# Kernel tuning notes

Hardware: AMD Instinct MI355X
Metric: run time of the kernel (lower is better)

The kernel has to match this reference:

```python
import jax, jax.numpy as jnp
import numpy as np

NUM_HEADS = 16
CHUNK = 64
RMS_EPS = 1.1920928955078125e-07  # torch.finfo(float32).eps, F.rms_norm default


def setup_inputs() -> dict:
    key = jax.random.key(0)
    k1, k2, k3 = jax.random.split(key, 3)
    B, S, D = 2, 4096, 2048
    x = jax.random.normal(k1, (B, S, D), dtype=jnp.float32)
    w_in = jax.random.normal(k2, (5 * D, D), dtype=jnp.float32) * 0.02
    w_out = jax.random.normal(k3, (D, D), dtype=jnp.float32) * 0.02
    return {"x": x, "w_in": w_in, "w_out": w_out}


def _forward(x, w_in, w_out):
    B, S, D = x.shape
    H, hd, C = NUM_HEADS, D // NUM_HEADS, CHUNK
    proj = x @ w_in.T                              # [B,S,5D]
    q, k, v, a, g = jnp.split(proj, 5, axis=-1)
    rs = lambda t: t.reshape(B, S, H, hd)
    q, k, v, a, g = map(rs, (q, k, v, a, g))
    # rms_norm over head_dim, no learned weight
    q = q * jax.lax.rsqrt(jnp.mean(q * q, axis=-1, keepdims=True) + RMS_EPS)
    k = jnp.tanh(k)
    a = jnp.clip(jax.nn.sigmoid(a + 2.0), 0.6, 0.9995)
    u = k * v                                      # updates, float32
    NC = S // C
    # [NC, B, C, H, hd] so lax.scan iterates over chunks
    a_r = a.reshape(B, NC, C, H, hd).transpose(1, 0, 2, 3, 4)
    u_r = u.reshape(B, NC, C, H, hd).transpose(1, 0, 2, 3, 4)

    def step(state, au):
        a_c, u_c = au                              # [B,C,H,hd]
        prefix = jnp.cumprod(a_c, axis=1)
        acc = jnp.cumsum(u_c / jnp.maximum(prefix, 1e-6), axis=1)
        states = prefix * (state[:, None] + acc)   # [B,C,H,hd]
        return states[:, -1], states

    state0 = jnp.zeros((B, H, hd), dtype=jnp.float32)
    _, mem = jax.lax.scan(step, state0, (a_r, u_r))  # [NC,B,C,H,hd]
    memory = mem.transpose(1, 0, 2, 3, 4).reshape(B, S, H, hd)
    gate = jax.nn.sigmoid(g)
    y = gate * (q * memory) + (1.0 - gate) * v
    return y.reshape(B, S, D) @ w_out.T


def reference(x, w_in, w_out):
    return _forward(x, w_in, w_out)
```

## Files before the change

### kernel.cpp

```cpp
#include <hip/hip_runtime.h>
#include <cstdint>
#include <cstddef>

typedef unsigned short u16;
typedef __bf16 bf16x8 __attribute__((ext_vector_type(8)));
typedef unsigned int u32;
typedef u32 u32x4 __attribute__((ext_vector_type(4)));
typedef float f32x4v __attribute__((ext_vector_type(4)));

#define BB 2
#define SS 4096
#define DD 2048
#define HH 16
#define HD 128
#define CC 64
#define NC 64
#define D5 10240
#define RMS_EPS 1.1920928955078125e-07f

__device__ __forceinline__ u16 f2bf(float f) {
  uint32_t x = __float_as_uint(f);
  uint32_t r = (x + 0x7fffu + ((x >> 16) & 1u)) >> 16;
  return (u16)r;
}
__device__ __forceinline__ float bf2f(u16 u) {
  return __uint_as_float(((uint32_t)u) << 16);
}
__device__ __forceinline__ float fast_sigmoid(float x) {
  return 1.0f / (1.0f + __expf(-x));
}
__device__ __forceinline__ float fast_tanh(float x) {
  return 1.0f - 2.0f / (__expf(2.0f * x) + 1.0f);
}

__global__ void cvt_bf16x8_kernel(const f32x4v* __restrict__ src,
                                  u32x4* __restrict__ dst, int n8) {
  int i = blockIdx.x * blockDim.x + threadIdx.x;
  int stride = gridDim.x * blockDim.x;
  for (; i < n8; i += stride) {
    f32x4v a = src[2 * i];
    f32x4v b = src[2 * i + 1];
    u32x4 o;
    o.x = (u32)f2bf(a.x) | ((u32)f2bf(a.y) << 16);
    o.y = (u32)f2bf(a.z) | ((u32)f2bf(a.w) << 16);
    o.z = (u32)f2bf(b.x) | ((u32)f2bf(b.y) << 16);
    o.w = (u32)f2bf(b.z) | ((u32)f2bf(b.w) << 16);
    dst[i] = o;
  }
}

template <typename OutT>
__global__ __launch_bounds__(512, 2) void gemm_bt(const u16* __restrict__ A,
                                                  const u16* __restrict__ B,
                                                  OutT* __restrict__ C,
                                                  int M, int N, int K) {
  __shared__ u16 lds[65536];

  const int tid = threadIdx.x;
  const int wave = tid >> 6;
  const int lane = tid & 63;

  const int nwg = (int)gridDim.x;
  const int bid = (int)blockIdx.x;
  const int bswz = (bid & 7) * (nwg >> 3) + (bid >> 3);
  const int Mt = M >> 8;
  const int m0 = (bswz % Mt) << 8;
  const int n0 = (bswz / Mt) << 8;

  const int wm = (wave >> 2) << 7;
  const int wn = (wave & 3) << 6;

  const int s_r = tid >> 3;
  const int s_ls = (tid & 7) ^ (s_r & 7);
  const u16* Ast = A + (size_t)(m0 + s_r) * K + s_ls * 8;
  const u16* Bst = B + (size_t)(n0 + s_r) * K + s_ls * 8;
  const int s_lb = wave * 512;

  const int fr = lane & 15;
  const int fg = lane >> 4;
  const int fx = lane & 7;
  const int psk0 = ((0 + fg) ^ fx) * 8;
  const int psk1 = ((4 + fg) ^ fx) * 8;
  const int aro = (wm + fr) * 64;
  const int bro = 16384 + (wn + fr) * 64;

  f32x4v acc[8][4] = {};
  bf16x8 afr[4][2];
  bf16x8 bfr[2][2][2];
  const int NT = K >> 6;

#define BARF()                              \
  do {                                      \
    asm volatile("" ::: "memory");          \
    __builtin_amdgcn_s_barrier();           \
    asm volatile("" ::: "memory");          \
  } while (0)

#define STAGE(GB, LB, H, KT)                                                    \
  do {                                                                          \
    const u16* g_ = (GB) + (size_t)((H) * 128) * K + (KT) * 64;                 \
    __builtin_amdgcn_global_load_lds(                                           \
        (__attribute__((address_space(1))) void*)(u16*)g_,                      \
        (__attribute__((address_space(3))) void*)&lds[(LB) + (H) * 8192 + s_lb],\
        16, 0, 0);                                                              \
    __builtin_amdgcn_global_load_lds(                                           \
        (__attribute__((address_space(1))) void*)(u16*)(g_ + (size_t)64 * K),   \
        (__attribute__((address_space(3))) void*)&lds[(LB) + (H) * 8192 + 4096 + s_lb], \
        16, 0, 0);                                                              \
  } while (0)

#define LOADA(BO, MH)                                             \
  do {                                                            \
    _Pragma("unroll") for (int mf = 0; mf < 4; ++mf) {            \
      const int ab_ = (BO) + aro + (MH) * 4096 + mf * 1024;       \
      afr[mf][0] = *(const bf16x8*)&lds[ab_ + psk0];              \
      afr[mf][1] = *(const bf16x8*)&lds[ab_ + psk1];              \
    }                                                             \
  } while (0)

#define LOADB(BO, NH)                                             \
  do {                                                            \
    _Pragma("unroll") for (int nf = 0; nf < 2; ++nf) {            \
      const int bb_ = (BO) + bro + (NH) * 2048 + nf * 1024;       \
      bfr[NH][nf][0] = *(const bf16x8*)&lds[bb_ + psk0];          \
      bfr[NH][nf][1] = *(const bf16x8*)&lds[bb_ + psk1];          \
    }                                                             \
  } while (0)

#define MMAQ(MH, NH)                                                          \
  do {                                                                        \
    __builtin_amdgcn_s_setprio(1);                                            \
    _Pragma("unroll") for (int mf = 0; mf < 4; ++mf)                          \
        _Pragma("unroll") for (int nf = 0; nf < 2; ++nf) {                    \
      acc[(MH) * 4 + mf][(NH) * 2 + nf] =                                     \
          __builtin_amdgcn_mfma_f32_16x16x32_bf16(                            \
              afr[mf][0], bfr[NH][nf][0], acc[(MH) * 4 + mf][(NH) * 2 + nf],  \
              0, 0, 0);                                                       \
      acc[(MH) * 4 + mf][(NH) * 2 + nf] =                                     \
          __builtin_amdgcn_mfma_f32_16x16x32_bf16(                            \
              afr[mf][1], bfr[NH][nf][1], acc[(MH) * 4 + mf][(NH) * 2 + nf],  \
              0, 0, 0);                                                       \
    }                                                                         \
    __builtin_amdgcn_s_setprio(0);                                            \
  } while (0)

  STAGE(Ast, 0, 0, 0);
  STAGE(Ast, 0, 1, 0);
  STAGE(Bst, 16384, 0, 0);
  STAGE(Bst, 16384, 1, 0);
  {
    const int k1 = (NT > 1) ? 1 : 0;
    STAGE(Ast, 32768, 0, k1);
    STAGE(Ast, 32768, 1, k1);
    STAGE(Bst, 49152, 0, k1);
    STAGE(Bst, 49152, 1, k1);
  }
  asm volatile("s_waitcnt vmcnt(8)" ::: "memory");
  BARF();

  for (int t = 0; t < NT; ++t) {
    const int bo = (t & 1) << 15;
    const int t2 = (t + 2 < NT) ? t + 2 : NT - 1;

    LOADA(bo, 0);
    LOADB(bo, 0);
    LOADB(bo, 1);
    MMAQ(0, 0);
    MMAQ(0, 1);
    LOADA(bo, 1);
    MMAQ(1, 1);
    __builtin_amdgcn_sched_barrier(0);
    BARF();

    STAGE(Ast, bo, 0, t2);
    STAGE(Bst, bo + 16384, 0, t2);
    STAGE(Ast, bo, 1, t2);
    STAGE(Bst, bo + 16384, 1, t2);
    MMAQ(1, 0);
    asm volatile("s_waitcnt vmcnt(8)" ::: "memory");
    BARF();
  }

  asm volatile("s_waitcnt vmcnt(0)" ::: "memory");
  BARF();

  const int ccol = lane & 15;
  const int crow = (lane >> 4) << 2;
  if constexpr (sizeof(OutT) == 2) {
    u16* wlds = &lds[wave * 8192];
#pragma unroll
    for (int am = 0; am < 8; ++am) {
#pragma unroll
      for (int an = 0; an < 4; ++an) {
        const int col = ((an >> 1) << 5) + ((an & 1) << 4) + ccol;
        const int cch = col >> 3, cre = col & 7;
#pragma unroll
        for (int r = 0; r < 4; ++r) {
          const int row = ((am >> 2) << 6) + ((am & 3) << 4) + crow + r;
          wlds[row * 64 + ((cch ^ (row & 7)) << 3) + cre] =
              f2bf(acc[am][an][r]);
        }
      }
    }
#pragma unroll
    for (int i = 0; i < 16; ++i) {
      const int row = i * 8 + (lane >> 3);
      const int ch = lane & 7;
      const u32x4 vv = *(const u32x4*)&wlds[row * 64 + (((ch) ^ (row & 7)) << 3)];
      *(u32x4*)(C + (size_t)(m0 + wm + row) * N + (n0 + wn + ch * 8)) = vv;
    }
  } else {
#pragma unroll
    for (int am = 0; am < 8; ++am) {
      const size_t r0 = (size_t)(m0 + wm + ((am >> 2) << 6) + ((am & 3) << 4) + crow);
#pragma unroll
      for (int an = 0; an < 4; ++an) {
        const size_t c0 = (size_t)(n0 + wn + ((an >> 1) << 5) + ((an & 1) << 4) + ccol);
#pragma unroll
        for (int r = 0; r < 4; ++r) {
          OutT* Cp = C + (r0 + r) * (size_t)N + c0;
          *Cp = acc[am][an][r];
        }
      }
    }
  }
#undef BARF
#undef STAGE
#undef LOADA
#undef LOADB
#undef MMAQ
}

__global__ __launch_bounds__(64) void scan_chunk(const u16* __restrict__ proj,
                                                 float* __restrict__ Pc,
                                                 float* __restrict__ Lc) {
  const int idx = blockIdx.x;
  const int h = idx & (HH - 1);
  const int c = (idx >> 4) & (NC - 1);
  const int b = idx >> 10;
  const int lane = threadIdx.x;

  const size_t row0 = (size_t)(b * SS + c * CC) * D5 + h * HD;

  float p0 = 1.0f, a0 = 0.0f, p1 = 1.0f, a1 = 0.0f;
  for (int t = 0; t < CC; ++t) {
    const size_t rp = row0 + (size_t)t * D5;
    float k0 = bf2f(proj[rp + DD + lane]);
    float k1 = bf2f(proj[rp + DD + lane + 64]);
    float v0 = bf2f(proj[rp + 2 * DD + lane]);
    float v1 = bf2f(proj[rp + 2 * DD + lane + 64]);
    float ar0 = bf2f(proj[rp + 3 * DD + lane]);
    float ar1 = bf2f(proj[rp + 3 * DD + lane + 64]);
    float aa0 = fminf(fmaxf(fast_sigmoid(ar0 + 2.0f), 0.6f), 0.9995f);
    float aa1 = fminf(fmaxf(fast_sigmoid(ar1 + 2.0f), 0.6f), 0.9995f);
    p0 *= aa0;
    p1 *= aa1;
    a0 += fast_tanh(k0) * v0 / fmaxf(p0, 1e-6f);
    a1 += fast_tanh(k1) * v1 / fmaxf(p1, 1e-6f);
  }
  const size_t ci = ((size_t)(b * NC + c) * HH + h) * HD;
  Pc[ci + lane] = p0;
  Pc[ci + lane + 64] = p1;
  Lc[ci + lane] = p0 * a0;
  Lc[ci + lane + 64] = p1 * a1;
}

__global__ void scan_carry(const float* __restrict__ Pc, const float* __restrict__ Lc,
                           float* __restrict__ Sin) {
  const int t = blockIdx.x * blockDim.x + threadIdx.x;
  const int b = t >> 11;
  const int hd = t & (DD - 1);
  float state = 0.0f;
  for (int c = 0; c < NC; ++c) {
    const size_t i = (size_t)(b * NC + c) * DD + hd;
    Sin[i] = state;
    state = Pc[i] * state + Lc[i];
  }
}

__global__ __launch_bounds__(64) void finalize_y(const u16* __restrict__ proj,
                                                 const float* __restrict__ Sin,
                                                 u16* __restrict__ y) {
  const int idx = blockIdx.x;
  const int h = idx & (HH - 1);
  const int c = (idx >> 4) & (NC - 1);
  const int b = idx >> 10;
  const int lane = threadIdx.x;

  const size_t row0 = (size_t)(b * SS + c * CC) * D5 + h * HD;
  const size_t out0 = (size_t)(b * SS + c * CC) * DD + h * HD;
  const size_t sinb = (size_t)(b * NC + c) * DD + h * HD;
  const float sin0 = Sin[sinb + lane];
  const float sin1 = Sin[sinb + lane + 64];

  float p0 = 1.0f, a0 = 0.0f, p1 = 1.0f, a1 = 0.0f;
  for (int t = 0; t < CC; ++t) {
    const size_t rp = row0 + (size_t)t * D5;
    const float q0 = bf2f(proj[rp + lane]);
    const float q1 = bf2f(proj[rp + lane + 64]);
    const float k0 = bf2f(proj[rp + DD + lane]);
    const float k1 = bf2f(proj[rp + DD + lane + 64]);
    const float v0 = bf2f(proj[rp + 2 * DD + lane]);
    const float v1 = bf2f(proj[rp + 2 * DD + lane + 64]);
    const float ar0 = bf2f(proj[rp + 3 * DD + lane]);
    const float ar1 = bf2f(proj[rp + 3 * DD + lane + 64]);
    const float g0 = bf2f(proj[rp + 4 * DD + lane]);
    const float g1 = bf2f(proj[rp + 4 * DD + lane + 64]);

    const float aa0 = fminf(fmaxf(fast_sigmoid(ar0 + 2.0f), 0.6f), 0.9995f);
    const float aa1 = fminf(fmaxf(fast_sigmoid(ar1 + 2.0f), 0.6f), 0.9995f);
    p0 *= aa0;
    p1 *= aa1;
    a0 += fast_tanh(k0) * v0 / fmaxf(p0, 1e-6f);
    a1 += fast_tanh(k1) * v1 / fmaxf(p1, 1e-6f);
    const float mem0 = p0 * (sin0 + a0);
    const float mem1 = p1 * (sin1 + a1);

    float ss = q0 * q0 + q1 * q1;
#pragma unroll
    for (int m = 32; m; m >>= 1) ss += __shfl_xor(ss, m);
    const float rn = rsqrtf(ss * (1.0f / 128.0f) + RMS_EPS);

    const float gt0 = fast_sigmoid(g0);
    const float gt1 = fast_sigmoid(g1);
    y[out0 + (size_t)t * DD + lane] = f2bf(gt0 * (q0 * rn * mem0) + (1.0f - gt0) * v0);
    y[out0 + (size_t)t * DD + lane + 64] = f2bf(gt1 * (q1 * rn * mem1) + (1.0f - gt1) * v1);
  }
}

extern "C" void kernel_launch(void* const* d_in, const int* in_sizes, int n_in,
                              void* d_out, int out_size, void* d_ws, size_t ws_size,
                              hipStream_t stream) {
  const float* x = (const float*)d_in[0];
  const float* w_in = (const float*)d_in[1];
  const float* w_out = (const float*)d_in[2];
  float* out = (float*)d_out;

  char* ws = (char*)d_ws;
  size_t off = 0;
  auto alloc = [&](size_t bytes) -> void* {
    void* p = ws + off;
    off += (bytes + 255) & ~(size_t)255;
    return p;
  };
  const size_t nBS = (size_t)BB * SS;
  u16* projb = (u16*)alloc(nBS * D5 * 2);
  u16* xb    = (u16*)alloc(nBS * DD * 2);
  u16* wib   = (u16*)alloc((size_t)D5 * DD * 2);
  u16* wob   = (u16*)alloc((size_t)DD * DD * 2);
  float* Pc  = (float*)alloc((size_t)BB * NC * DD * 4);
  float* Lc  = (float*)alloc((size_t)BB * NC * DD * 4);
  float* Sin = (float*)alloc((size_t)BB * NC * DD * 4);
  u16* yb = xb;
  (void)in_sizes; (void)n_in; (void)out_size;

  if (off > ws_size) return;

  cvt_bf16x8_kernel<<<1024, 256, 0, stream>>>((const f32x4v*)x, (u32x4*)xb,
                                              (int)(nBS * DD / 8));
  cvt_bf16x8_kernel<<<1024, 256, 0, stream>>>((const f32x4v*)w_in, (u32x4*)wib,
                                              (int)((size_t)D5 * DD / 8));
  cvt_bf16x8_kernel<<<1024, 256, 0, stream>>>((const f32x4v*)w_out, (u32x4*)wob,
                                              (int)((size_t)DD * DD / 8));

  gemm_bt<u16><<<dim3(32 * 40), 512, 0, stream>>>(xb, wib, projb, 8192, 10240, 2048);

  scan_chunk<<<BB * NC * HH, 64, 0, stream>>>(projb, Pc, Lc);

  scan_carry<<<16, 256, 0, stream>>>(Pc, Lc, Sin);

  finalize_y<<<BB * NC * HH, 64, 0, stream>>>(projb, Sin, yb);

  gemm_bt<float><<<dim3(32 * 8), 512, 0, stream>>>(yb, wob, out, 8192, 2048, 2048);
}
```

Measured before the change: 657.5 us.

## Load GEMM B operand directly from global into double-buffered registers, halve LDS

```diff
diff --git a/kernel.cpp b/kernel.cpp
--- a/kernel.cpp
+++ b/kernel.cpp
@@ -54,7 +54,7 @@
                                                   const u16* __restrict__ B,
                                                   OutT* __restrict__ C,
                                                   int M, int N, int K) {
-  __shared__ u16 lds[65536];
+  __shared__ u16 lds[32768];
 
   const int tid = threadIdx.x;
   const int wave = tid >> 6;
@@ -73,7 +73,6 @@
   const int s_r = tid >> 3;
   const int s_ls = (tid & 7) ^ (s_r & 7);
   const u16* Ast = A + (size_t)(m0 + s_r) * K + s_ls * 8;
-  const u16* Bst = B + (size_t)(n0 + s_r) * K + s_ls * 8;
   const int s_lb = wave * 512;
 
   const int fr = lane & 15;
@@ -82,11 +81,17 @@
   const int psk0 = ((0 + fg) ^ fx) * 8;
   const int psk1 = ((4 + fg) ^ fx) * 8;
   const int aro = (wm + fr) * 64;
-  const int bro = 16384 + (wn + fr) * 64;
+
+  const u16* bq[2][2];
+#pragma unroll
+  for (int NH = 0; NH < 2; ++NH)
+#pragma unroll
+    for (int nf = 0; nf < 2; ++nf)
+      bq[NH][nf] = B + (size_t)(n0 + wn + NH * 32 + nf * 16 + fr) * K + fg * 8;
 
   f32x4v acc[8][4] = {};
-  bf16x8 afr[4][2];
-  bf16x8 bfr[2][2][2];
+  bf16x8 afr[2][2];
+  bf16x8 bA[2][2][2], bB[2][2][2];
   const int NT = K >> 6;
 
 #define BARF()                              \
@@ -109,76 +114,70 @@
         16, 0, 0);                                                              \
   } while (0)
 
-#define LOADA(BO, MH)                                             \
-  do {                                                            \
-    _Pragma("unroll") for (int mf = 0; mf < 4; ++mf) {            \
-      const int ab_ = (BO) + aro + (MH) * 4096 + mf * 1024;       \
-      afr[mf][0] = *(const bf16x8*)&lds[ab_ + psk0];              \
-      afr[mf][1] = *(const bf16x8*)&lds[ab_ + psk1];              \
-    }                                                             \
-  } while (0)
-
-#define LOADB(BO, NH)                                             \
-  do {                                                            \
-    _Pragma("unroll") for (int nf = 0; nf < 2; ++nf) {            \
-      const int bb_ = (BO) + bro + (NH) * 2048 + nf * 1024;       \
-      bfr[NH][nf][0] = *(const bf16x8*)&lds[bb_ + psk0];          \
-      bfr[NH][nf][1] = *(const bf16x8*)&lds[bb_ + psk1];          \
-    }                                                             \
-  } while (0)
-
-#define MMAQ(MH, NH)                                                          \
+#define ISSUE_B(DST, KT)                                                \
+  do {                                                                  \
+    _Pragma("unroll") for (int NH = 0; NH < 2; ++NH)                    \
+      _Pragma("unroll") for (int nf = 0; nf < 2; ++nf) {                \
+        DST[NH][nf][0] = *(const bf16x8*)(bq[NH][nf] + (KT) * 64);      \
+        DST[NH][nf][1] = *(const bf16x8*)(bq[NH][nf] + (KT) * 64 + 32); \
+      }                                                                 \
+  } while (0)
+
+#define LOADA2(BO, MH, MP)                                              \
+  do {                                                                  \
+    _Pragma("unroll") for (int mf2 = 0; mf2 < 2; ++mf2) {               \
+      const int ab_ = (BO) + aro + (MH) * 4096 + (MP) * 2048 + mf2 * 1024; \
+      afr[mf2][0] = *(const bf16x8*)&lds[ab_ + psk0];                   \
+      afr[mf2][1] = *(const bf16x8*)&lds[ab_ + psk1];                   \
+    }                                                                   \
+  } while (0)
+
+#define MM8(MH, MP, NH, BC)                                                   \
   do {                                                                        \
     __builtin_amdgcn_s_setprio(1);                                            \
-    _Pragma("unroll") for (int mf = 0; mf < 4; ++mf)                          \
+    _Pragma("unroll") for (int mf2 = 0; mf2 < 2; ++mf2)                       \
         _Pragma("unroll") for (int nf = 0; nf < 2; ++nf) {                    \
-      acc[(MH) * 4 + mf][(NH) * 2 + nf] =                                     \
-          __builtin_amdgcn_mfma_f32_16x16x32_bf16(                            \
-              afr[mf][0], bfr[NH][nf][0], acc[(MH) * 4 + mf][(NH) * 2 + nf],  \
-              0, 0, 0);                                                       \
-      acc[(MH) * 4 + mf][(NH) * 2 + nf] =                                     \
-          __builtin_amdgcn_mfma_f32_16x16x32_bf16(                            \
-              afr[mf][1], bfr[NH][nf][1], acc[(MH) * 4 + mf][(NH) * 2 + nf],  \
-              0, 0, 0);                                                       \
+      f32x4v* ac_ = &acc[(MH) * 4 + (MP) * 2 + mf2][(NH) * 2 + nf];           \
+      *ac_ = __builtin_amdgcn_mfma_f32_16x16x32_bf16(                         \
+          afr[mf2][0], BC[NH][nf][0], *ac_, 0, 0, 0);                         \
+      *ac_ = __builtin_amdgcn_mfma_f32_16x16x32_bf16(                         \
+          afr[mf2][1], BC[NH][nf][1], *ac_, 0, 0, 0);                         \
     }                                                                         \
     __builtin_amdgcn_s_setprio(0);                                            \
   } while (0)
 
+#define ITER(T, BC, BN)                                                 \
+  do {                                                                  \
+    const int bo_ = ((T) & 1) << 14;                                    \
+    const int tn_ = ((T) + 1 < NT) ? (T) + 1 : NT - 1;                  \
+    const int t2_ = ((T) + 2 < NT) ? (T) + 2 : NT - 1;                  \
+    ISSUE_B(BN, tn_);                                                   \
+    LOADA2(bo_, 0, 0); MM8(0, 0, 0, BC); MM8(0, 0, 1, BC);              \
+    LOADA2(bo_, 0, 1); MM8(0, 1, 0, BC); MM8(0, 1, 1, BC);              \
+    LOADA2(bo_, 1, 0); MM8(1, 0, 0, BC); MM8(1, 0, 1, BC);              \
+    LOADA2(bo_, 1, 1); MM8(1, 1, 0, BC); MM8(1, 1, 1, BC);              \
+    __builtin_amdgcn_sched_barrier(0);                                  \
+    BARF();                                                             \
+    STAGE(Ast, bo_, 0, t2_);                                            \
+    STAGE(Ast, bo_, 1, t2_);                                            \
+    asm volatile("s_waitcnt vmcnt(12)" ::: "memory");                   \
+    BARF();                                                             \
+  } while (0)
+
   STAGE(Ast, 0, 0, 0);
   STAGE(Ast, 0, 1, 0);
-  STAGE(Bst, 16384, 0, 0);
-  STAGE(Bst, 16384, 1, 0);
   {
     const int k1 = (NT > 1) ? 1 : 0;
-    STAGE(Ast, 32768, 0, k1);
-    STAGE(Ast, 32768, 1, k1);
-    STAGE(Bst, 49152, 0, k1);
-    STAGE(Bst, 49152, 1, k1);
-  }
-  asm volatile("s_waitcnt vmcnt(8)" ::: "memory");
+    STAGE(Ast, 16384, 0, k1);
+    STAGE(Ast, 16384, 1, k1);
+  }
+  ISSUE_B(bA, 0);
+  asm volatile("s_waitcnt vmcnt(0)" ::: "memory");
   BARF();
 
-  for (int t = 0; t < NT; ++t) {
-    const int bo = (t & 1) << 15;
-    const int t2 = (t + 2 < NT) ? t + 2 : NT - 1;
-
-    LOADA(bo, 0);
-    LOADB(bo, 0);
-    LOADB(bo, 1);
-    MMAQ(0, 0);
-    MMAQ(0, 1);
-    LOADA(bo, 1);
-    MMAQ(1, 1);
-    __builtin_amdgcn_sched_barrier(0);
-    BARF();
-
-    STAGE(Ast, bo, 0, t2);
-    STAGE(Bst, bo + 16384, 0, t2);
-    STAGE(Ast, bo, 1, t2);
-    STAGE(Bst, bo + 16384, 1, t2);
-    MMAQ(1, 0);
-    asm volatile("s_waitcnt vmcnt(8)" ::: "memory");
-    BARF();
+  for (int t = 0; t < NT; t += 2) {
+    ITER(t, bA, bB);
+    ITER(t + 1, bB, bA);
   }
 
   asm volatile("s_waitcnt vmcnt(0)" ::: "memory");
@@ -187,27 +186,32 @@
   const int ccol = lane & 15;
   const int crow = (lane >> 4) << 2;
   if constexpr (sizeof(OutT) == 2) {
-    u16* wlds = &lds[wave * 8192];
-#pragma unroll
-    for (int am = 0; am < 8; ++am) {
-#pragma unroll
-      for (int an = 0; an < 4; ++an) {
-        const int col = ((an >> 1) << 5) + ((an & 1) << 4) + ccol;
-        const int cch = col >> 3, cre = col & 7;
-#pragma unroll
-        for (int r = 0; r < 4; ++r) {
-          const int row = ((am >> 2) << 6) + ((am & 3) << 4) + crow + r;
-          wlds[row * 64 + ((cch ^ (row & 7)) << 3) + cre] =
-              f2bf(acc[am][an][r]);
+    u16* wlds = &lds[wave * 4096];
+#pragma unroll
+    for (int half = 0; half < 2; ++half) {
+#pragma unroll
+      for (int am4 = 0; am4 < 4; ++am4) {
+        const int am = half * 4 + am4;
+#pragma unroll
+        for (int an = 0; an < 4; ++an) {
+          const int col = ((an >> 1) << 5) + ((an & 1) << 4) + ccol;
+          const int cch = col >> 3, cre = col & 7;
+#pragma unroll
+          for (int r = 0; r < 4; ++r) {
+            const int row = (am4 << 4) + crow + r;
+            wlds[row * 64 + ((cch ^ (row & 7)) << 3) + cre] =
+                f2bf(acc[am][an][r]);
+          }
         }
       }
-    }
-#pragma unroll
-    for (int i = 0; i < 16; ++i) {
-      const int row = i * 8 + (lane >> 3);
-      const int ch = lane & 7;
-      const u32x4 vv = *(const u32x4*)&wlds[row * 64 + (((ch) ^ (row & 7)) << 3)];
-      *(u32x4*)(C + (size_t)(m0 + wm + row) * N + (n0 + wn + ch * 8)) = vv;
+#pragma unroll
+      for (int i = 0; i < 8; ++i) {
+        const int row = i * 8 + (lane >> 3);
+        const int ch = lane & 7;
+        const u32x4 vv = *(const u32x4*)&wlds[row * 64 + ((ch ^ (row & 7)) << 3)];
+        *(u32x4*)(C + (size_t)(m0 + wm + half * 64 + row) * N + (n0 + wn + ch * 8)) = vv;
+      }
+      __builtin_amdgcn_s_barrier();
     }
   } else {
 #pragma unroll
@@ -226,9 +230,10 @@
   }
 #undef BARF
 #undef STAGE
-#undef LOADA
-#undef LOADB
-#undef MMAQ
+#undef ISSUE_B
+#undef LOADA2
+#undef MM8
+#undef ITER
 }
 
 __global__ __launch_bounds__(64) void scan_chunk(const u16* __restrict__ proj,
```

New measurement: 863.6 us. 31.4% more time.
